# Performance work log

Measured on AMD Instinct MI355X. Metric: run time of the kernel, lower is better.

Reference implementation:

```python
import jax, jax.numpy as jnp
import numpy as np

HID = 64; H = 2; D = 32; L = 2; G = 64; F_IN = 771
NA = 120000; NE = 60000; E0 = 1500000; E1 = 1000000; E2 = 1000000


def _seg_mean(x, seg, n):
    s = jax.ops.segment_sum(x, seg, num_segments=n)
    c = jax.ops.segment_sum(jnp.ones((x.shape[0], 1), x.dtype), seg, num_segments=n)
    return s / jnp.maximum(c, 1.0)


def setup_inputs() -> dict:
    ks = jax.random.split(jax.random.key(0), 32)
    r = lambda i, s: 0.02 * jax.random.normal(ks[i], s, jnp.float32)
    z = lambda s: jnp.zeros(s, jnp.float32)
    inp = {}
    inp['x_argument'] = jax.random.normal(ks[0], (NA, F_IN), jnp.float32)
    inp['x_evidence'] = jax.random.normal(ks[1], (NE, F_IN), jnp.float32)
    inp['Win'] = r(2, (2, F_IN, HID)); inp['b_in'] = z((2, HID))
    inp['Wk'] = r(3, (L, 2, HID, HID)); inp['bk'] = z((L, 2, HID))
    inp['Wq'] = r(4, (L, 2, HID, HID)); inp['bq'] = z((L, 2, HID))
    inp['Wv'] = r(5, (L, 2, HID, HID)); inp['bv'] = z((L, 2, HID))
    inp['Wa'] = r(6, (L, 2, HID, HID)); inp['ba'] = z((L, 2, HID))
    inp['skip'] = jnp.ones((L, 2), jnp.float32)
    inp['Watt'] = r(7, (L, 3, H, D, D)); inp['Wmsg'] = r(8, (L, 3, H, D, D))
    inp['prel'] = jnp.ones((L, 3, H), jnp.float32)
    inp['Wnews'] = r(9, (384, HID)); inp['bnews'] = z((HID,))
    inp['Wdeb'] = r(10, (HID, HID)); inp['bdeb'] = z((HID,))
    inp['Wqm'] = r(11, (HID, HID)); inp['bqm'] = z((HID,))
    inp['Wkm'] = r(12, (HID, HID)); inp['bkm'] = z((HID,))
    inp['Wvm'] = r(13, (HID, HID)); inp['bvm'] = z((HID,))
    inp['Wom'] = r(14, (HID, HID)); inp['bom'] = z((HID,))
    inp['Wc1'] = r(15, (2 * HID, 64)); inp['bc1'] = z((64,))
    inp['Wc2'] = r(16, (64, 1)); inp['bc2'] = z((1,))
    inp['e0_src'] = jax.random.randint(ks[17], (E0,), 0, NA)
    inp['e0_dst'] = jax.random.randint(ks[18], (E0,), 0, NA)
    inp['e1_src'] = jax.random.randint(ks[19], (E1,), 0, NE)
    inp['e1_dst'] = jax.random.randint(ks[20], (E1,), 0, NA)
    inp['e2_src'] = jax.random.randint(ks[21], (E2,), 0, NA)
    inp['e2_dst'] = jax.random.randint(ks[22], (E2,), 0, NE)
    inp['batch_arg'] = jnp.sort(jax.random.randint(ks[23], (NA,), 0, G))
    return inp


def reference(x_argument, x_evidence, Win, b_in, Wk, bk, Wq, bq, Wv, bv, Wa, ba,
              skip, Watt, Wmsg, prel, Wnews, bnews, Wdeb, bdeb,
              Wqm, bqm, Wkm, bkm, Wvm, bvm, Wom, bom, Wc1, bc1, Wc2, bc2,
              e0_src, e0_dst, e1_src, e1_dst, e2_src, e2_dst, batch_arg):
    # Claim embedding from RAW features (slice 384:768), pooled per graph.
    claim_raw = _seg_mean(x_argument[:, 384:768], batch_arg, G)
    # Per-node-type input projection + ReLU. type 0 = argument, 1 = evidence.
    xs = [jax.nn.relu(x_argument @ Win[0] + b_in[0]),
          jax.nn.relu(x_evidence @ Win[1] + b_in[1])]
    # (src_type, dst_type, src_idx, dst_idx) for each heterogeneous edge type.
    edges = [(0, 0, e0_src, e0_dst), (1, 0, e1_src, e1_dst), (0, 1, e2_src, e2_dst)]
    scale = 1.0 / jnp.sqrt(jnp.float32(D))
    for l in range(L):  # HGTConv stack
        Kt = [(xs[t] @ Wk[l, t] + bk[l, t]).reshape(-1, H, D) for t in range(2)]
        Qt = [(xs[t] @ Wq[l, t] + bq[l, t]).reshape(-1, H, D) for t in range(2)]
        Vt = [(xs[t] @ Wv[l, t] + bv[l, t]).reshape(-1, H, D) for t in range(2)]
        buf = {0: [], 1: []}
        for e, (s, d, src, dst) in enumerate(edges):
            k2 = jnp.einsum('ehd,hdf->ehf', Kt[s][src], Watt[l, e])  # relation key transform
            v2 = jnp.einsum('ehd,hdf->ehf', Vt[s][src], Wmsg[l, e])  # relation msg transform
            sc = (Qt[d][dst] * k2).sum(-1) * prel[l, e] * scale      # (E, H)
            buf[d].append((sc, dst, v2))
        new_xs = []
        for d in range(2):
            n = xs[d].shape[0]
            sc = jnp.concatenate([b[0] for b in buf[d]], 0)
            dst = jnp.concatenate([b[1] for b in buf[d]], 0)
            v2 = jnp.concatenate([b[2] for b in buf[d]], 0)
            # segment softmax over all incoming edges of each destination node
            m = jax.ops.segment_max(sc, dst, num_segments=n)
            ex = jnp.exp(sc - m[dst])
            den = jax.ops.segment_sum(ex, dst, num_segments=n)
            alpha = ex / den[dst]
            agg = jax.ops.segment_sum(alpha[..., None] * v2, dst, num_segments=n).reshape(n, HID)
            out = jax.nn.gelu(agg, approximate=False) @ Wa[l, d] + ba[l, d]
            beta = jax.nn.sigmoid(skip[l, d])
            new_xs.append(beta * out + (1.0 - beta) * xs[d])
        xs = new_xs
    graph_emb = _seg_mean(xs[0], batch_arg, G)
    eF = claim_raw @ Wnews + bnews          # (G, HID)
    g = graph_emb @ Wdeb + bdeb             # (G, HID)
    # MultiheadAttention with query len 1 and key len 1: softmax over a single
    # key is identically 1, so attn_out == out_proj(v_proj(g)) exactly
    # (Wqm/bqm/Wkm/bkm receive exactly zero gradient, matching torch).
    v = g @ Wvm + bvm
    attn_out = v @ Wom + bom
    h = jax.nn.relu(jnp.concatenate([g, attn_out], -1) @ Wc1 + bc1)  # dropout is eval-mode identity
    return h @ Wc2 + bc2  # (G, 1)
```

## Files before the change

kernel.cpp:

```cpp
#include <hip/hip_runtime.h>
#include <math.h>

#define N0 120000
#define N1 60000
#define E0N 1500000
#define E1N 1000000
#define E2N 1000000
#define FIN 771
#define NG 64
#define KSTEPS_IN 25

#define GB0 ((N0 + 127) / 128)
#define GB1 ((N1 + 127) / 128)
#define AB0 ((N0 + 3) / 4)
#define AB1 ((N1 + 3) / 4)
#define SB0 ((N0 + 1023) / 1024)
#define SB1 ((N1 + 1023) / 1024)
#define PREPB 70

#define Q0O   ((size_t)0)
#define KV00O ((size_t)N0 * 128)
#define KV02O ((size_t)N0 * 256)
#define Q1O   ((size_t)N0 * 384)
#define KV11O ((size_t)N0 * 384 + (size_t)N1 * 128)

#define SKV 256.0f
#define INV_SKV 0.00390625f

typedef __attribute__((ext_vector_type(8))) short short8;
typedef __attribute__((ext_vector_type(4))) float f32x4;
typedef __attribute__((ext_vector_type(2))) float f32x2;
typedef float f32x4u __attribute__((ext_vector_type(4), aligned(4)));
typedef __attribute__((ext_vector_type(4))) unsigned short ushort4v;
typedef unsigned short ushort;
typedef unsigned char uchar;

__device__ __forceinline__ float gelu_f(float v) {
    return 0.5f * v * (1.f + erff(v * 0.70710678118654752f));
}
__device__ __forceinline__ ushort f2b(float f) {
    union { float f; unsigned u; } v; v.f = f;
    unsigned u = v.u;
    return (ushort)((u + 0x7FFFu + ((u >> 16) & 1u)) >> 16);
}
__device__ __forceinline__ float b2f(ushort h) {
    union { unsigned u; float f; } v; v.u = ((unsigned)h) << 16; return v.f;
}
__device__ __forceinline__ float lo16(unsigned u) {
    union { unsigned x; float f; } v; v.x = u << 16; return v.f;
}
__device__ __forceinline__ float hi16(unsigned u) {
    union { unsigned x; float f; } v; v.x = u & 0xFFFF0000u; return v.f;
}
__device__ __forceinline__ int asi(float f) { union { float f; int i; } v; v.f = f; return v.i; }
__device__ __forceinline__ float asf(int i) { union { int i; float f; } v; v.i = i; return v.f; }

__device__ __forceinline__ void proj_phase(
    const ushort* xls, char* scratch, int type, int l, int w, int lane, int tid,
    int r0b, int nrows,
    const ushort* __restrict__ Wpack, const float* __restrict__ bpack,
    uchar* __restrict__ projAll)
{
    short8 bfr[2][2];
    #pragma unroll
    for (int ksp = 0; ksp < 2; ++ksp)
        #pragma unroll
        for (int rb = 0; rb < 2; ++rb)
            bfr[ksp][rb] = *(const short8*)&xls[(w * 32 + rb * 16 + (lane & 15)) * 72
                                                + ksp * 32 + (lane >> 4) * 8];
    const int sbase = l * 8 + (type ? 5 : 0);
    const int c0b = (lane >> 4) * 4;
    const int ngroups = type ? 2 : 3;

    for (int grp = 0; grp < ngroups; ++grp) {
        const int s0 = (grp == 0) ? 0 : (grp * 2 - 1);
        const int nsl = (grp == 0) ? 1 : 2;
        for (int si = 0; si < nsl; ++si) {
            const int slot = s0 + si;
            const ushort* Wp = Wpack + (size_t)(sbase + slot) * 4096;
            const float* bias = bpack + (size_t)(sbase + slot) * 64;
            f32x4 acc[2][4] = {};
            #pragma unroll
            for (int ksp = 0; ksp < 2; ++ksp) {
                const ushort* wb = Wp + ksp * 2048 + lane * 8;
                #pragma unroll
                for (int cg = 0; cg < 4; ++cg) {
                    short8 afr = *(const short8*)&wb[cg * 512];
                    acc[0][cg] = __builtin_amdgcn_mfma_f32_16x16x32_bf16(afr, bfr[ksp][0], acc[0][cg], 0, 0, 0);
                    acc[1][cg] = __builtin_amdgcn_mfma_f32_16x16x32_bf16(afr, bfr[ksp][1], acc[1][cg], 0, 0, 0);
                }
            }
            #pragma unroll
            for (int rb = 0; rb < 2; ++rb) {
                int lrow = w * 32 + rb * 16 + (lane & 15);
                const int sw = (lrow & 7) << 4;
                #pragma unroll
                for (int cg = 0; cg < 4; ++cg) {
                    int c = cg * 16 + c0b;
                    float v0 = acc[rb][cg][0] + bias[c + 0];
                    float v1 = acc[rb][cg][1] + bias[c + 1];
                    float v2 = acc[rb][cg][2] + bias[c + 2];
                    float v3 = acc[rb][cg][3] + bias[c + 3];
                    if (grp == 0) {
                        ushort4v o;
                        o[0] = f2b(v0); o[1] = f2b(v1); o[2] = f2b(v2); o[3] = f2b(v3);
                        *(ushort4v*)(scratch + lrow * 128 + ((c * 2) ^ sw)) = o;
                    } else {
                        int wrd = __builtin_amdgcn_cvt_pk_fp8_f32(v0 * SKV, v1 * SKV, 0, 0);
                        wrd = __builtin_amdgcn_cvt_pk_fp8_f32(v2 * SKV, v3 * SKV, wrd, 1);
                        *(int*)(scratch + lrow * 128 + ((((c >> 2) << 3) + (si << 2)) ^ sw)) = wrd;
                    }
                }
            }
        }
        __syncthreads();
        size_t ooff;
        if (grp == 0) ooff = type ? Q1O : Q0O;
        else if (grp == 1) ooff = type ? KV11O : KV00O;
        else ooff = KV02O;
        char* outg = (char*)projAll + ooff + (size_t)r0b * 128;
        #pragma unroll
        for (int q = 0; q < 4; ++q) {
            int off = q * 4096 + tid * 16;
            int row = off >> 7;
            int inner = off & 127;
            if (r0b + row < nrows)
                *(uint4*)(outg + off) =
                    *(const uint4*)(scratch + row * 128 + (inner ^ ((row & 7) << 4)));
        }
        __syncthreads();
    }
}

__global__ __launch_bounds__(256) void inproj_proj_kernel(
    const float* __restrict__ xa, const float* __restrict__ xe,
    const ushort* __restrict__ Wpin, const float* __restrict__ b_in,
    ushort* __restrict__ xs0, ushort* __restrict__ xs1,
    const ushort* __restrict__ Wpack, const float* __restrict__ bpack,
    uchar* __restrict__ projAll)
{
    __shared__ ushort xls[128 * 72];
    __shared__ char scratch[16384];
    const int bx = blockIdx.x;
    const int type = (bx >= GB0) ? 1 : 0;
    const float* __restrict__ x = type ? xe : xa;
    const int nrows = type ? N1 : N0;
    const ushort* __restrict__ Wp = Wpin + (type ? (size_t)KSTEPS_IN * 2048 : 0);
    const float* __restrict__ bias = b_in + type * 64;
    ushort* __restrict__ out = type ? xs1 : xs0;

    const int tid = threadIdx.x, w = tid >> 6, lane = tid & 63;
    const int r0b = (type ? bx - GB0 : bx) * 128;

    const int rA = min(r0b + w * 32 + (lane & 15), nrows - 1);
    const int rB = min(r0b + w * 32 + 16 + (lane & 15), nrows - 1);
    const float* __restrict__ xA = x + (size_t)rA * FIN + (lane >> 4) * 8;
    const float* __restrict__ xB = x + (size_t)rB * FIN + (lane >> 4) * 8;

    f32x4 acc[2][4] = {};
    f32x4u cb[3][4];
    cb[0][0] = *(const f32x4u*)xA;        cb[0][1] = *(const f32x4u*)(xA + 4);
    cb[0][2] = *(const f32x4u*)xB;        cb[0][3] = *(const f32x4u*)(xB + 4);
    cb[1][0] = *(const f32x4u*)(xA + 32); cb[1][1] = *(const f32x4u*)(xA + 36);
    cb[1][2] = *(const f32x4u*)(xB + 32); cb[1][3] = *(const f32x4u*)(xB + 36);

    #pragma unroll
    for (int ks = 0; ks < 24; ++ks) {
        if (ks + 2 < 24) {
            const float* pA = xA + (ks + 2) * 32;
            const float* pB = xB + (ks + 2) * 32;
            cb[(ks + 2) % 3][0] = *(const f32x4u*)pA;
            cb[(ks + 2) % 3][1] = *(const f32x4u*)(pA + 4);
            cb[(ks + 2) % 3][2] = *(const f32x4u*)pB;
            cb[(ks + 2) % 3][3] = *(const f32x4u*)(pB + 4);
        }
        const int cur = ks % 3;
        short8 bA, bB;
        #pragma unroll
        for (int j = 0; j < 4; ++j) {
            bA[j]     = (short)f2b(cb[cur][0][j]);
            bA[j + 4] = (short)f2b(cb[cur][1][j]);
            bB[j]     = (short)f2b(cb[cur][2][j]);
            bB[j + 4] = (short)f2b(cb[cur][3][j]);
        }
        const ushort* wb = Wp + (size_t)ks * 2048 + lane * 8;
        #pragma unroll
        for (int cg = 0; cg < 4; ++cg) {
            short8 afr = *(const short8*)&wb[cg * 512];
            acc[0][cg] = __builtin_amdgcn_mfma_f32_16x16x32_bf16(afr, bA, acc[0][cg], 0, 0, 0);
            acc[1][cg] = __builtin_amdgcn_mfma_f32_16x16x32_bf16(afr, bB, acc[1][cg], 0, 0, 0);
        }
    }
    {
        short8 bA = {}, bB = {};
        if ((lane >> 4) == 0) {
            const float* tA = x + (size_t)rA * FIN + 768;
            const float* tB = x + (size_t)rB * FIN + 768;
            bA[0] = (short)f2b(tA[0]); bA[1] = (short)f2b(tA[1]); bA[2] = (short)f2b(tA[2]);
            bB[0] = (short)f2b(tB[0]); bB[1] = (short)f2b(tB[1]); bB[2] = (short)f2b(tB[2]);
        }
        const ushort* wb = Wp + (size_t)24 * 2048 + lane * 8;
        #pragma unroll
        for (int cg = 0; cg < 4; ++cg) {
            short8 afr = *(const short8*)&wb[cg * 512];
            acc[0][cg] = __builtin_amdgcn_mfma_f32_16x16x32_bf16(afr, bA, acc[0][cg], 0, 0, 0);
            acc[1][cg] = __builtin_amdgcn_mfma_f32_16x16x32_bf16(afr, bB, acc[1][cg], 0, 0, 0);
        }
    }
    const int c0b = (lane >> 4) * 4;
    #pragma unroll
    for (int rb = 0; rb < 2; ++rb) {
        int lrow = w * 32 + rb * 16 + (lane & 15);
        int r = r0b + lrow;
        #pragma unroll
        for (int cg = 0; cg < 4; ++cg) {
            int c = cg * 16 + c0b;
            ushort4v h;
            h[0] = f2b(fmaxf(acc[rb][cg][0] + bias[c + 0], 0.f));
            h[1] = f2b(fmaxf(acc[rb][cg][1] + bias[c + 1], 0.f));
            h[2] = f2b(fmaxf(acc[rb][cg][2] + bias[c + 2], 0.f));
            h[3] = f2b(fmaxf(acc[rb][cg][3] + bias[c + 3], 0.f));
            *(ushort4v*)&xls[lrow * 72 + c] = h;
            if (r < nrows) *(ushort4v*)&out[(size_t)r * 64 + c] = h;
        }
    }
    __syncthreads();
    proj_phase(xls, scratch, type, 0, w, lane, tid, r0b, nrows, Wpack, bpack, projAll);
}

template <int DO_PROJ>
__global__ __launch_bounds__(256) void epi_kernel(
    const float* __restrict__ agg0, const float* __restrict__ agg1,
    const ushort* __restrict__ WaPack, const float* __restrict__ ba,
    ushort* __restrict__ xs0, ushort* __restrict__ xs1,
    const float* __restrict__ skip, int l,
    const ushort* __restrict__ Wpack, const float* __restrict__ bpack,
    uchar* __restrict__ projAll)
{
    __shared__ ushort xls[DO_PROJ ? 128 * 72 : 64];
    __shared__ char scratch[DO_PROJ ? 16384 : 64];
    const int bx = blockIdx.x;
    const int type = (bx >= GB0) ? 1 : 0;
    const float* __restrict__ in = type ? agg1 : agg0;
    ushort* __restrict__ xs = type ? xs1 : xs0;
    const int nrows = type ? N1 : N0;
    const ushort* __restrict__ Wp = WaPack + (size_t)(l * 2 + type) * 4096;
    const float* __restrict__ bias = ba + (size_t)(l * 2 + type) * 64;
    const float beta = 1.f / (1.f + __expf(-skip[l * 2 + type]));

    const int tid = threadIdx.x, w = tid >> 6, lane = tid & 63;
    const int r0b = (type ? bx - GB0 : bx) * 128;
    const int r0 = r0b + w * 32;
    f32x4 acc[2][4] = {};
    #pragma unroll
    for (int ksp = 0; ksp < 2; ++ksp) {
        short8 bfr[2];
        #pragma unroll
        for (int rb = 0; rb < 2; ++rb) {
            int gr = min(r0 + rb * 16 + (lane & 15), nrows - 1);
            const float* src = in + (size_t)gr * 64 + ksp * 32 + (lane >> 4) * 8;
            float4 f0 = *(const float4*)src;
            float4 f1 = *(const float4*)(src + 4);
            short8 t;
            t[0] = (short)f2b(gelu_f(f0.x)); t[1] = (short)f2b(gelu_f(f0.y));
            t[2] = (short)f2b(gelu_f(f0.z)); t[3] = (short)f2b(gelu_f(f0.w));
            t[4] = (short)f2b(gelu_f(f1.x)); t[5] = (short)f2b(gelu_f(f1.y));
            t[6] = (short)f2b(gelu_f(f1.z)); t[7] = (short)f2b(gelu_f(f1.w));
            bfr[rb] = t;
        }
        const ushort* wb = Wp + ksp * 2048 + lane * 8;
        #pragma unroll
        for (int cg = 0; cg < 4; ++cg) {
            short8 afr = *(const short8*)&wb[cg * 512];
            acc[0][cg] = __builtin_amdgcn_mfma_f32_16x16x32_bf16(afr, bfr[0], acc[0][cg], 0, 0, 0);
            acc[1][cg] = __builtin_amdgcn_mfma_f32_16x16x32_bf16(afr, bfr[1], acc[1][cg], 0, 0, 0);
        }
    }
    const int c0b = (lane >> 4) * 4;
    #pragma unroll
    for (int rb = 0; rb < 2; ++rb) {
        int lrow = w * 32 + rb * 16 + (lane & 15);
        int r = r0b + lrow;
        int gr = min(r, nrows - 1);
        #pragma unroll
        for (int cg = 0; cg < 4; ++cg) {
            int c = cg * 16 + c0b;
            ushort4v xo = *(const ushort4v*)&xs[(size_t)gr * 64 + c];
            ushort4v h;
            h[0] = f2b(beta * (acc[rb][cg][0] + bias[c + 0]) + (1.f - beta) * b2f(xo[0]));
            h[1] = f2b(beta * (acc[rb][cg][1] + bias[c + 1]) + (1.f - beta) * b2f(xo[1]));
            h[2] = f2b(beta * (acc[rb][cg][2] + bias[c + 2]) + (1.f - beta) * b2f(xo[2]));
            h[3] = f2b(beta * (acc[rb][cg][3] + bias[c + 3]) + (1.f - beta) * b2f(xo[3]));
            if (DO_PROJ) *(ushort4v*)&xls[lrow * 72 + c] = h;
            if (r < nrows) *(ushort4v*)&xs[(size_t)r * 64 + c] = h;
        }
    }
    if (DO_PROJ) {
        __syncthreads();
        proj_phase(xls, scratch, type, l + 1, w, lane, tid, r0b, nrows, Wpack, bpack, projAll);
    }
}

__global__ __launch_bounds__(256) void prep_zero_kernel(
    const float* __restrict__ Wq, const float* __restrict__ bq,
    const float* __restrict__ Wk, const float* __restrict__ bk,
    const float* __restrict__ Wv, const float* __restrict__ bv,
    const float* __restrict__ Watt, const float* __restrict__ Wmsg,
    const float* __restrict__ prel, const float* __restrict__ Win,
    const float* __restrict__ Wa,
    ushort* __restrict__ Wpack, float* __restrict__ bpack,
    ushort* __restrict__ Wpin, ushort* __restrict__ WaPack,
    int* __restrict__ c0, int* __restrict__ c1,
    int* __restrict__ gs, int* __restrict__ gc)
{
    __shared__ float WF[4096];
    const int b = blockIdx.x;
    const int tid = threadIdx.x;
    if (b >= PREPB) {
        int i = (b - PREPB) * 256 + tid;
        if (i < N0) c0[i] = 0;
        else if (i < N0 + N1) c1[i - N0] = 0;
        else if (i < N0 + N1 + NG * 64) gs[i - N0 - N1] = 0;
        else if (i < N0 + N1 + NG * 64 + NG) gc[i - N0 - N1 - NG * 64] = 0;
        return;
    }
    if (b < 16) {
        const int l = b >> 3;
        const int slot = b & 7;
        const float SCALE = 0.17677669529663689f;
        ushort* outW = Wpack + (size_t)(l * 8 + slot) * 4096;
        float* outB = bpack + (size_t)(l * 8 + slot) * 64;
        const float *Wsrc = 0, *bsrc = 0, *A = 0, *prelE = 0;
        int copy = 0;
        switch (slot) {
            case 0: Wsrc = Wq + (l*2+0)*4096; bsrc = bq + (l*2+0)*64; copy = 1; break;
            case 5: Wsrc = Wq + (l*2+1)*4096; bsrc = bq + (l*2+1)*64; copy = 1; break;
            case 1: Wsrc = Wk + (l*2+0)*4096; bsrc = bk + (l*2+0)*64; A = Watt + (l*3+0)*2048; prelE = prel + l*6 + 0; break;
            case 2: Wsrc = Wv + (l*2+0)*4096; bsrc = bv + (l*2+0)*64; A = Wmsg + (l*3+0)*2048; break;
            case 3: Wsrc = Wk + (l*2+0)*4096; bsrc = bk + (l*2+0)*64; A = Watt + (l*3+2)*2048; prelE = prel + l*6 + 4; break;
            case 4: Wsrc = Wv + (l*2+0)*4096; bsrc = bv + (l*2+0)*64; A = Wmsg + (l*3+2)*2048; break;
            case 6: Wsrc = Wk + (l*2+1)*4096; bsrc = bk + (l*2+1)*64; A = Watt + (l*3+1)*2048; prelE = prel + l*6 + 2; break;
            case 7: Wsrc = Wv + (l*2+1)*4096; bsrc = bv + (l*2+1)*64; A = Wmsg + (l*3+1)*2048; break;
        }
        if (copy) {
            for (int idx = tid; idx < 4096; idx += 256) WF[idx] = Wsrc[idx];
            if (tid < 64) outB[tid] = bsrc[tid];
        } else {
            for (int idx = tid; idx < 4096; idx += 256) {
                int k = idx >> 6, c = idx & 63, h = c >> 5, f = c & 31;
                float s = 0.f;
                for (int d = 0; d < 32; ++d)
                    s += Wsrc[k * 64 + h * 32 + d] * A[(h * 32 + d) * 32 + f];
                if (prelE) s *= prelE[h] * SCALE;
                WF[idx] = s;
            }
            if (tid < 64) {
                int h = tid >> 5, f = tid & 31;
                float s = 0.f;
                for (int d = 0; d < 32; ++d)
                    s += bsrc[h * 32 + d] * A[(h * 32 + d) * 32 + f];
                if (prelE) s *= prelE[h] * SCALE;
                outB[tid] = s;
            }
        }
        __syncthreads();
        for (int idx = tid; idx < 4096; idx += 256) {
            int ksp = idx >> 11, rem = idx & 2047;
            int cg = rem >> 9, rem2 = rem & 511;
            int lane = rem2 >> 3, j = rem2 & 7;
            int k = ksp * 32 + (lane >> 4) * 8 + j;
            int c = cg * 16 + (lane & 15);
            outW[idx] = f2b(WF[k * 64 + c]);
        }
    } else if (b < 16 + 2 * KSTEPS_IN) {
        const int pb = b - 16;
        const int type = pb / KSTEPS_IN, ks = pb % KSTEPS_IN;
        const float* W = Win + (size_t)type * FIN * 64;
        ushort* out = Wpin + (size_t)pb * 2048;
        for (int idx = tid; idx < 2048; idx += 256) {
            int cg = idx >> 9, rem = idx & 511, lane = rem >> 3, j = rem & 7;
            int k = ks * 32 + (lane >> 4) * 8 + j;
            int c = cg * 16 + (lane & 15);
            out[idx] = f2b((k < FIN) ? W[(size_t)k * 64 + c] : 0.f);
        }
    } else {
        const int mb = b - 16 - 2 * KSTEPS_IN;
        const float* W = Wa + (size_t)mb * 4096;
        ushort* o = WaPack + (size_t)mb * 4096;
        for (int idx = tid; idx < 4096; idx += 256) {
            int ksp = idx >> 11, rem = idx & 2047;
            int cg = rem >> 9, rem2 = rem & 511;
            int lane = rem2 >> 3, j = rem2 & 7;
            int k = ksp * 32 + (lane >> 4) * 8 + j;
            int c = cg * 16 + (lane & 15);
            o[idx] = f2b(W[k * 64 + c]);
        }
    }
}

__global__ void hist_all_kernel(
    const int* __restrict__ e0d, const int* __restrict__ e1d, const int* __restrict__ e2d,
    int* __restrict__ cnt0, int* __restrict__ cnt1)
{
    const int Q0 = E0N / 4, Q1 = E1N / 4, Q2 = E2N / 4;
    const int total = Q0 + Q1 + Q2;
    for (int i = blockIdx.x * blockDim.x + threadIdx.x; i < total; i += gridDim.x * blockDim.x) {
        int4 d;
        int* cnt;
        if (i < Q0) { d = *(const int4*)(e0d + i * 4); cnt = cnt0; }
        else if (i < Q0 + Q1) { d = *(const int4*)(e1d + (i - Q0) * 4); cnt = cnt0; }
        else { d = *(const int4*)(e2d + (i - Q0 - Q1) * 4); cnt = cnt1; }
        atomicAdd(&cnt[d.x], 1);
        atomicAdd(&cnt[d.y], 1);
        atomicAdd(&cnt[d.z], 1);
        atomicAdd(&cnt[d.w], 1);
    }
}

__global__ __launch_bounds__(256) void scan1_all_kernel(
    int* __restrict__ cnt0, int* __restrict__ cnt1,
    int* __restrict__ off0, int* __restrict__ off1,
    int* __restrict__ bsA, int* __restrict__ bsB)
{
    __shared__ int sa[256], sb[256];
    const int tid = threadIdx.x;
    const int b = blockIdx.x;
    int* cnt; int n; int* off; int* bsum; int lb;
    if (b < SB0) { cnt = cnt0; n = N0; off = off0; bsum = bsA; lb = b; }
    else { cnt = cnt1; n = N1; off = off1; bsum = bsB; lb = b - SB0; }
    const int base = lb * 1024 + tid * 4;
    int v[4];
    int run = 0;
    #pragma unroll
    for (int i = 0; i < 4; ++i) {
        int x = (base + i < n) ? cnt[base + i] : 0;
        run += x; v[i] = run;
    }
    #pragma unroll
    for (int i = 0; i < 4; ++i)
        if (base + i < n) cnt[base + i] = 0;
    sa[tid] = run;
    __syncthreads();
    int* src = sa; int* dst = sb;
    for (int d = 1; d < 256; d <<= 1) {
        int x = src[tid];
        if (tid >= d) x += src[tid - d];
        dst[tid] = x;
        __syncthreads();
        int* t = src; src = dst; dst = t;
    }
    int excl = src[tid] - run;
    #pragma unroll
    for (int i = 0; i < 4; ++i)
        if (base + i < n) off[base + i + 1] = excl + v[i];
    if (tid == 255) bsum[lb] = src[255];
}

__global__ __launch_bounds__(256) void scan3_all_kernel(
    int* __restrict__ off0, int* __restrict__ off1,
    const int* __restrict__ bsA, const int* __restrict__ bsB)
{
    __shared__ int red[256];
    const int b = blockIdx.x;
    const int tid = threadIdx.x;
    int* off; const int* bsum; int n; int lb;
    if (b < SB0) { off = off0; bsum = bsA; n = N0; lb = b; }
    else { off = off1; bsum = bsB; n = N1; lb = b - SB0; }
    int partial = 0;
    for (int i = tid; i < lb; i += 256) partial += bsum[i];
    red[tid] = partial;
    __syncthreads();
    #pragma unroll
    for (int d = 128; d > 0; d >>= 1) {
        if (tid < d) red[tid] += red[tid + d];
        __syncthreads();
    }
    const int add = red[0];
    const int base = lb * 1024 + tid * 4;
    #pragma unroll
    for (int i = 0; i < 4; ++i)
        if (base + i < n) off[base + i + 1] += add;
    if (lb == 0 && tid == 0) off[0] = 0;
}

__global__ void scatter_all_kernel(
    const int* __restrict__ e0s, const int* __restrict__ e0d,
    const int* __restrict__ e1s, const int* __restrict__ e1d,
    const int* __restrict__ e2s, const int* __restrict__ e2d,
    const int* __restrict__ off0, const int* __restrict__ off1,
    int* __restrict__ cnt0, int* __restrict__ cnt1,
    int* __restrict__ rec0, int* __restrict__ rec1)
{
    const int Q0 = E0N / 4, Q1 = E1N / 4, Q2 = E2N / 4;
    const int total = Q0 + Q1 + Q2;
    for (int i = blockIdx.x * blockDim.x + threadIdx.x; i < total; i += gridDim.x * blockDim.x) {
        int4 d, sv;
        const int* off; int* cnt; int* rec; int tag;
        if (i < Q0) {
            d = *(const int4*)(e0d + i * 4); sv = *(const int4*)(e0s + i * 4);
            off = off0; cnt = cnt0; rec = rec0; tag = 0;
        } else if (i < Q0 + Q1) {
            int k = (i - Q0) * 4;
            d = *(const int4*)(e1d + k); sv = *(const int4*)(e1s + k);
            off = off0; cnt = cnt0; rec = rec0; tag = 1 << 20;
        } else {
            int k = (i - Q0 - Q1) * 4;
            d = *(const int4*)(e2d + k); sv = *(const int4*)(e2s + k);
            off = off1; cnt = cnt1; rec = rec1; tag = 0;
        }
        rec[off[d.x] + atomicAdd(&cnt[d.x], 1)] = sv.x | tag;
        rec[off[d.y] + atomicAdd(&cnt[d.y], 1)] = sv.y | tag;
        rec[off[d.z] + atomicAdd(&cnt[d.z], 1)] = sv.z | tag;
        rec[off[d.w] + atomicAdd(&cnt[d.w], 1)] = sv.w | tag;
    }
}

__global__ __launch_bounds__(256) void agg_fused(
    const int* __restrict__ off0, const int* __restrict__ rec0,
    const int* __restrict__ off1, const int* __restrict__ rec1,
    const uchar* __restrict__ projAll,
    float* __restrict__ agg0, float* __restrict__ agg1)
{
    const int bx = blockIdx.x;
    const int type = (bx >= AB0) ? 1 : 0;
    const int lane = threadIdx.x & 63;
    const int node = (type ? bx - AB0 : bx) * 4 + (threadIdx.x >> 6);
    const int ndst = type ? N1 : N0;
    if (node >= ndst) return;
    const int* __restrict__ off = type ? off1 : off0;
    const int* __restrict__ rec = type ? rec1 : rec0;
    const ushort* __restrict__ Q = (const ushort*)(projAll + (type ? Q1O : Q0O));
    const uchar* __restrict__ KVa = projAll + (type ? KV02O : KV00O);
    const uchar* __restrict__ KVb = projAll + (type ? KV02O : KV11O);
    float* __restrict__ outAgg = type ? agg1 : agg0;

    const int grp = lane >> 4;
    const int gi  = lane & 15;
    float q0, q1, q2, q3;
    {
        const unsigned* qp = (const unsigned*)(Q + (size_t)node * 64 + gi * 4);
        unsigned u0 = qp[0], u1 = qp[1];
        q0 = lo16(u0) * INV_SKV; q1 = hi16(u0) * INV_SKV;
        q2 = lo16(u1) * INV_SKV; q3 = hi16(u1) * INV_SKV;
    }
    const int s = off[node], e = off[node + 1];
    float den = 0.f, a0 = 0.f, a1 = 0.f, a2 = 0.f, a3 = 0.f;
    for (int j = s; j < e; j += 16) {
        bool v[4]; uint2 kv[4]; float p[4];
        #pragma unroll
        for (int q = 0; q < 4; ++q) {
            int jj = j + grp + q * 4;
            v[q] = jj < e;
            int r = rec[v[q] ? jj : s];
            const uchar* KV = (r & (1 << 20)) ? KVb : KVa;
            kv[q] = *(const uint2*)(KV + ((size_t)(unsigned)(r & 0xFFFFF) << 7) + gi * 8);
        }
        #pragma unroll
        for (int q = 0; q < 4; ++q) {
            f32x2 kA = __builtin_amdgcn_cvt_pk_f32_fp8(kv[q].x, 0);
            f32x2 kB = __builtin_amdgcn_cvt_pk_f32_fp8(kv[q].x, 1);
            p[q] = kA[0] * q0 + kA[1] * q1 + kB[0] * q2 + kB[1] * q3;
        }
        #pragma unroll
        for (int q = 0; q < 4; ++q) p[q] += asf(__builtin_amdgcn_ds_swizzle(asi(p[q]), 0x041F));
        #pragma unroll
        for (int q = 0; q < 4; ++q) p[q] += asf(__builtin_amdgcn_ds_swizzle(asi(p[q]), 0x081F));
        #pragma unroll
        for (int q = 0; q < 4; ++q) p[q] += asf(__builtin_amdgcn_ds_swizzle(asi(p[q]), 0x101F));
        #pragma unroll
        for (int q = 0; q < 4; ++q) {
            float wgt = v[q] ? __expf(p[q]) : 0.f;
            den += wgt;
            f32x2 vA = __builtin_amdgcn_cvt_pk_f32_fp8(kv[q].y, 0);
            f32x2 vB = __builtin_amdgcn_cvt_pk_f32_fp8(kv[q].y, 1);
            a0 = fmaf(wgt, vA[0], a0);
            a1 = fmaf(wgt, vA[1], a1);
            a2 = fmaf(wgt, vB[0], a2);
            a3 = fmaf(wgt, vB[1], a3);
        }
    }
    a0 += __shfl_xor(a0, 16); a0 += __shfl_xor(a0, 32);
    a1 += __shfl_xor(a1, 16); a1 += __shfl_xor(a1, 32);
    a2 += __shfl_xor(a2, 16); a2 += __shfl_xor(a2, 32);
    a3 += __shfl_xor(a3, 16); a3 += __shfl_xor(a3, 32);
    den += __shfl_xor(den, 16); den += __shfl_xor(den, 32);
    if (lane < 16) {
        float inv = (den > 0.f) ? 1.f / (den * SKV) : 0.f;
        float4 o;
        o.x = a0 * inv; o.y = a1 * inv; o.z = a2 * inv; o.w = a3 * inv;
        *(float4*)&outAgg[(size_t)node * 64 + gi * 4] = o;
    }
}

__global__ __launch_bounds__(256) void segsum_kernel(
    const ushort* __restrict__ xs, const int* __restrict__ seg, int n,
    float* __restrict__ gsum, int* __restrict__ gcnt)
{
    const int lane = threadIdx.x & 63;
    const int wid = blockIdx.x * 4 + (threadIdx.x >> 6);
    const int rbeg = wid * 256;
    if (rbeg >= n) return;
    const int rend = min(rbeg + 256, n);
    float s = 0.f;
    int cur = seg[rbeg];
    int run = 0;
    for (int r = rbeg; r < rend; ++r) {
        int sg = seg[r];
        if (sg != cur) {
            atomicAdd(&gsum[cur * 64 + lane], s);
            if (lane == 0) atomicAdd(&gcnt[cur], run);
            cur = sg; s = 0.f; run = 0;
        }
        s += b2f(xs[(size_t)r * 64 + lane]);
        run++;
    }
    atomicAdd(&gsum[cur * 64 + lane], s);
    if (lane == 0) atomicAdd(&gcnt[cur], run);
}

__global__ __launch_bounds__(256) void head_kernel(
    const float* __restrict__ gsum, const int* __restrict__ gcnt,
    const float* __restrict__ Wdeb, const float* __restrict__ bdeb,
    const float* __restrict__ Wvm, const float* __restrict__ bvm,
    const float* __restrict__ Wom, const float* __restrict__ bom,
    const float* __restrict__ Wc1, const float* __restrict__ bc1,
    const float* __restrict__ Wc2, const float* __restrict__ bc2,
    float* __restrict__ outp)
{
    __shared__ float A[4096], B[4096], C[4096];
    const int tid = threadIdx.x;
    for (int idx = tid; idx < 4096; idx += 256) {
        int g = idx >> 6;
        A[idx] = gsum[idx] / fmaxf((float)gcnt[g], 1.f);
    }
    __syncthreads();
    for (int idx = tid; idx < 4096; idx += 256) {
        int g = idx >> 6, c = idx & 63;
        float s = bdeb[c];
        for (int k = 0; k < 64; ++k) s = fmaf(A[g * 64 + k], Wdeb[k * 64 + c], s);
        B[idx] = s;
    }
    __syncthreads();
    for (int idx = tid; idx < 4096; idx += 256) {
        int g = idx >> 6, c = idx & 63;
        float s = bvm[c];
        for (int k = 0; k < 64; ++k) s = fmaf(B[g * 64 + k], Wvm[k * 64 + c], s);
        C[idx] = s;
    }
    __syncthreads();
    for (int idx = tid; idx < 4096; idx += 256) {
        int g = idx >> 6, c = idx & 63;
        float s = bom[c];
        for (int k = 0; k < 64; ++k) s = fmaf(C[g * 64 + k], Wom[k * 64 + c], s);
        A[idx] = s;
    }
    __syncthreads();
    for (int idx = tid; idx < 4096; idx += 256) {
        int g = idx >> 6, c = idx & 63;
        float s = bc1[c];
        for (int k = 0; k < 64; ++k) s = fmaf(B[g * 64 + k], Wc1[k * 64 + c], s);
        for (int k = 0; k < 64; ++k) s = fmaf(A[g * 64 + k], Wc1[(64 + k) * 64 + c], s);
        C[idx] = fmaxf(s, 0.f);
    }
    __syncthreads();
    if (tid < 64) {
        float s = bc2[0];
        for (int c = 0; c < 64; ++c) s = fmaf(C[tid * 64 + c], Wc2[c], s);
        outp[tid] = s;
    }
}

extern "C" void kernel_launch(void* const* d_in, const int* in_sizes, int n_in,
                              void* d_out, int out_size, void* d_ws, size_t ws_size,
                              hipStream_t stream)
{
    const float* x_arg = (const float*)d_in[0];
    const float* x_ev  = (const float*)d_in[1];
    const float* Win   = (const float*)d_in[2];
    const float* b_in  = (const float*)d_in[3];
    const float* Wk    = (const float*)d_in[4];
    const float* bk    = (const float*)d_in[5];
    const float* Wq    = (const float*)d_in[6];
    const float* bq    = (const float*)d_in[7];
    const float* Wv    = (const float*)d_in[8];
    const float* bv    = (const float*)d_in[9];
    const float* Wa    = (const float*)d_in[10];
    const float* ba    = (const float*)d_in[11];
    const float* skip  = (const float*)d_in[12];
    const float* Watt  = (const float*)d_in[13];
    const float* Wmsg  = (const float*)d_in[14];
    const float* prel  = (const float*)d_in[15];
    const float* Wdeb  = (const float*)d_in[18];
    const float* bdeb  = (const float*)d_in[19];
    const float* Wvm   = (const float*)d_in[24];
    const float* bvm   = (const float*)d_in[25];
    const float* Wom   = (const float*)d_in[26];
    const float* bom   = (const float*)d_in[27];
    const float* Wc1   = (const float*)d_in[28];
    const float* bc1   = (const float*)d_in[29];
    const float* Wc2   = (const float*)d_in[30];
    const float* bc2   = (const float*)d_in[31];
    const int* e0s = (const int*)d_in[32];
    const int* e0d = (const int*)d_in[33];
    const int* e1s = (const int*)d_in[34];
    const int* e1d = (const int*)d_in[35];
    const int* e2s = (const int*)d_in[36];
    const int* e2d = (const int*)d_in[37];
    const int* batch = (const int*)d_in[38];
    float* outp = (float*)d_out;

    char* w = (char*)d_ws;
    size_t o = 0;
    auto alloc = [&](size_t bytes) -> char* {
        char* p = w + o;
        o = (o + bytes + 255) & ~(size_t)255;
        return p;
    };
    ushort* xs0  = (ushort*)alloc((size_t)N0 * 64 * 2);
    ushort* xs1  = (ushort*)alloc((size_t)N1 * 64 * 2);
    uchar* projAll = (uchar*)alloc((size_t)N0 * 384 + (size_t)N1 * 256);
    float* agg0  = (float*)alloc((size_t)N0 * 64 * 4);
    float* agg1  = (float*)alloc((size_t)N1 * 64 * 4);
    int* off0 = (int*)alloc((size_t)(N0 + 1) * 4);
    int* off1 = (int*)alloc((size_t)(N1 + 1) * 4);
    int* cnt0 = (int*)alloc((size_t)N0 * 4);
    int* cnt1 = (int*)alloc((size_t)N1 * 4);
    int* rec0 = (int*)alloc((size_t)(E0N + E1N) * 4);
    int* rec1 = (int*)alloc((size_t)E2N * 4);
    int* bsA  = (int*)alloc(256 * 4);
    int* bsB  = (int*)alloc(256 * 4);
    ushort* Wpack = (ushort*)alloc((size_t)16 * 4096 * 2);
    float* bpack = (float*)alloc((size_t)16 * 64 * 4);
    ushort* Wpin = (ushort*)alloc((size_t)2 * KSTEPS_IN * 2048 * 2);
    ushort* WaPack = (ushort*)alloc((size_t)4 * 4096 * 2);
    float* gsum = (float*)alloc((size_t)NG * 64 * 4);
    int* gcnt = (int*)alloc((size_t)NG * 4);
    if (o > ws_size) return;

    const int ZB = (N0 + N1 + NG * 64 + NG + 255) / 256;

    prep_zero_kernel<<<PREPB + ZB, 256, 0, stream>>>(
        Wq, bq, Wk, bk, Wv, bv, Watt, Wmsg, prel, Win, Wa,
        Wpack, bpack, Wpin, WaPack, cnt0, cnt1, (int*)gsum, gcnt);
    hist_all_kernel<<<1024, 256, 0, stream>>>(e0d, e1d, e2d, cnt0, cnt1);
    scan1_all_kernel<<<SB0 + SB1, 256, 0, stream>>>(cnt0, cnt1, off0, off1, bsA, bsB);
    scan3_all_kernel<<<SB0 + SB1, 256, 0, stream>>>(off0, off1, bsA, bsB);
    scatter_all_kernel<<<1024, 256, 0, stream>>>(
        e0s, e0d, e1s, e1d, e2s, e2d, off0, off1, cnt0, cnt1, rec0, rec1);
    inproj_proj_kernel<<<GB0 + GB1, 256, 0, stream>>>(
        x_arg, x_ev, Wpin, b_in, xs0, xs1, Wpack, bpack, projAll);
    agg_fused<<<AB0 + AB1, 256, 0, stream>>>(off0, rec0, off1, rec1, projAll, agg0, agg1);
    epi_kernel<1><<<GB0 + GB1, 256, 0, stream>>>(
        agg0, agg1, WaPack, ba, xs0, xs1, skip, 0, Wpack, bpack, projAll);
    agg_fused<<<AB0 + AB1, 256, 0, stream>>>(off0, rec0, off1, rec1, projAll, agg0, agg1);
    epi_kernel<0><<<GB0 + GB1, 256, 0, stream>>>(
        agg0, agg1, WaPack, ba, xs0, xs1, skip, 1, Wpack, bpack, projAll);
    {
        int waves = (N0 + 255) / 256;
        segsum_kernel<<<(waves + 3) / 4, 256, 0, stream>>>(xs0, batch, N0, gsum, gcnt);
    }
    head_kernel<<<1, 256, 0, stream>>>(gsum, gcnt, Wdeb, bdeb, Wvm, bvm, Wom, bom,
                                       Wc1, bc1, Wc2, bc2, outp);
}
```

Baseline: 974.9 us.

## Stage input-projection rows through LDS with coalesced loads, halve block rows

The input projection kernel now loads each block's contiguous slab of fp32 input rows with fully coalesced vector loads, converts them to bf16, and stores them in a shared-memory tile before the MFMA loop. Previously each lane read strided 32-byte chunks per row directly from global memory. Blocks now cover 64 rows instead of 128, and proj_phase is templated on the row count. The aim is better DRAM efficiency on the large 771-wide input read and more blocks in flight. The cost is about 99KB of LDS per block, which limits occupancy, plus an extra sync.

Measured after the change: 1.040 ms. 1.07x slower.

```diff
diff --git a/kernel.cpp b/kernel.cpp
--- a/kernel.cpp
+++ b/kernel.cpp
@@ -12,6 +12,8 @@
 
 #define GB0 ((N0 + 127) / 128)
 #define GB1 ((N1 + 127) / 128)
+#define GB064 (N0 / 64)
+#define GB164 ((N1 + 63) / 64)
 #define AB0 ((N0 + 3) / 4)
 #define AB1 ((N1 + 3) / 4)
 #define SB0 ((N0 + 1023) / 1024)
@@ -55,18 +57,20 @@
 __device__ __forceinline__ int asi(float f) { union { float f; int i; } v; v.f = f; return v.i; }
 __device__ __forceinline__ float asf(int i) { union { int i; float f; } v; v.i = i; return v.f; }
 
+template <int NRB>
 __device__ __forceinline__ void proj_phase(
     const ushort* xls, char* scratch, int type, int l, int w, int lane, int tid,
     int r0b, int nrows,
     const ushort* __restrict__ Wpack, const float* __restrict__ bpack,
     uchar* __restrict__ projAll)
 {
-    short8 bfr[2][2];
+    const int ROWS = NRB * 64;
+    short8 bfr[2][NRB];
     #pragma unroll
     for (int ksp = 0; ksp < 2; ++ksp)
         #pragma unroll
-        for (int rb = 0; rb < 2; ++rb)
-            bfr[ksp][rb] = *(const short8*)&xls[(w * 32 + rb * 16 + (lane & 15)) * 72
+        for (int rb = 0; rb < NRB; ++rb)
+            bfr[ksp][rb] = *(const short8*)&xls[(w * 16 * NRB + rb * 16 + (lane & 15)) * 72
                                                 + ksp * 32 + (lane >> 4) * 8];
     const int sbase = l * 8 + (type ? 5 : 0);
     const int c0b = (lane >> 4) * 4;
@@ -79,20 +83,21 @@
             const int slot = s0 + si;
             const ushort* Wp = Wpack + (size_t)(sbase + slot) * 4096;
             const float* bias = bpack + (size_t)(sbase + slot) * 64;
-            f32x4 acc[2][4] = {};
+            f32x4 acc[NRB][4] = {};
             #pragma unroll
             for (int ksp = 0; ksp < 2; ++ksp) {
                 const ushort* wb = Wp + ksp * 2048 + lane * 8;
                 #pragma unroll
                 for (int cg = 0; cg < 4; ++cg) {
                     short8 afr = *(const short8*)&wb[cg * 512];
-                    acc[0][cg] = __builtin_amdgcn_mfma_f32_16x16x32_bf16(afr, bfr[ksp][0], acc[0][cg], 0, 0, 0);
-                    acc[1][cg] = __builtin_amdgcn_mfma_f32_16x16x32_bf16(afr, bfr[ksp][1], acc[1][cg], 0, 0, 0);
+                    #pragma unroll
+                    for (int rb = 0; rb < NRB; ++rb)
+                        acc[rb][cg] = __builtin_amdgcn_mfma_f32_16x16x32_bf16(afr, bfr[ksp][rb], acc[rb][cg], 0, 0, 0);
                 }
             }
             #pragma unroll
-            for (int rb = 0; rb < 2; ++rb) {
-                int lrow = w * 32 + rb * 16 + (lane & 15);
+            for (int rb = 0; rb < NRB; ++rb) {
+                int lrow = w * 16 * NRB + rb * 16 + (lane & 15);
                 const int sw = (lrow & 7) << 4;
                 #pragma unroll
                 for (int cg = 0; cg < 4; ++cg) {
@@ -120,7 +125,7 @@
         else ooff = KV02O;
         char* outg = (char*)projAll + ooff + (size_t)r0b * 128;
         #pragma unroll
-        for (int q = 0; q < 4; ++q) {
+        for (int q = 0; q < ROWS / 32; ++q) {
             int off = q * 4096 + tid * 16;
             int row = off >> 7;
             int inner = off & 127;
@@ -139,10 +144,12 @@
     const ushort* __restrict__ Wpack, const float* __restrict__ bpack,
     uchar* __restrict__ projAll)
 {
-    __shared__ ushort xls[128 * 72];
-    __shared__ char scratch[16384];
+    __shared__ union {
+        ushort xt[64 * 772];
+        struct { ushort xls[64 * 72]; char scratch[8192]; } pp;
+    } sm;
     const int bx = blockIdx.x;
-    const int type = (bx >= GB0) ? 1 : 0;
+    const int type = (bx >= GB064) ? 1 : 0;
     const float* __restrict__ x = type ? xe : xa;
     const int nrows = type ? N1 : N0;
     const ushort* __restrict__ Wp = Wpin + (type ? (size_t)KSTEPS_IN * 2048 : 0);
@@ -150,82 +157,85 @@
     ushort* __restrict__ out = type ? xs1 : xs0;
 
     const int tid = threadIdx.x, w = tid >> 6, lane = tid & 63;
-    const int r0b = (type ? bx - GB0 : bx) * 128;
-
-    const int rA = min(r0b + w * 32 + (lane & 15), nrows - 1);
-    const int rB = min(r0b + w * 32 + 16 + (lane & 15), nrows - 1);
-    const float* __restrict__ xA = x + (size_t)rA * FIN + (lane >> 4) * 8;
-    const float* __restrict__ xB = x + (size_t)rB * FIN + (lane >> 4) * 8;
-
-    f32x4 acc[2][4] = {};
-    f32x4u cb[3][4];
-    cb[0][0] = *(const f32x4u*)xA;        cb[0][1] = *(const f32x4u*)(xA + 4);
-    cb[0][2] = *(const f32x4u*)xB;        cb[0][3] = *(const f32x4u*)(xB + 4);
-    cb[1][0] = *(const f32x4u*)(xA + 32); cb[1][1] = *(const f32x4u*)(xA + 36);
-    cb[1][2] = *(const f32x4u*)(xB + 32); cb[1][3] = *(const f32x4u*)(xB + 36);
-
+    const int r0b = (type ? bx - GB064 : bx) * 64;
+
+    const float* __restrict__ src = x + (size_t)r0b * FIN;
+    const int nelem = (min(r0b + 64, nrows) - r0b) * FIN;
+    int e = tid * 4;
+    int row = (e >= FIN) ? 1 : 0;
+    int col = e - row * FIN;
+    for (int b = 0; b < 6; ++b) {
+        f32x4u v[8];
+        #pragma unroll
+        for (int i = 0; i < 8; ++i) {
+            int ee = e + i * 1024;
+            v[i] = (ee < nelem) ? *(const f32x4u*)(src + ee) : (f32x4u){};
+        }
+        #pragma unroll
+        for (int i = 0; i < 8; ++i) {
+            #pragma unroll
+            for (int j = 0; j < 4; ++j) {
+                int cc = col + j, rr = row;
+                if (cc >= FIN) { cc -= FIN; ++rr; }
+                sm.xt[rr * 772 + cc] = f2b(v[i][j]);
+            }
+            row += 1; col += 253;
+            if (col >= FIN) { col -= FIN; row += 1; }
+        }
+        e += 8192;
+    }
+    if (tid < 48) {
+        int ee = 49152 + tid * 4;
+        f32x4u v = (ee < nelem) ? *(const f32x4u*)(src + ee) : (f32x4u){};
+        int cc = ee - 63 * FIN;
+        #pragma unroll
+        for (int j = 0; j < 4; ++j) sm.xt[63 * 772 + cc + j] = f2b(v[j]);
+    }
+    __syncthreads();
+
+    const int mrow = w * 16 + (lane & 15);
+    f32x4 acc[4] = {};
     #pragma unroll
     for (int ks = 0; ks < 24; ++ks) {
-        if (ks + 2 < 24) {
-            const float* pA = xA + (ks + 2) * 32;
-            const float* pB = xB + (ks + 2) * 32;
-            cb[(ks + 2) % 3][0] = *(const f32x4u*)pA;
-            cb[(ks + 2) % 3][1] = *(const f32x4u*)(pA + 4);
-            cb[(ks + 2) % 3][2] = *(const f32x4u*)pB;
-            cb[(ks + 2) % 3][3] = *(const f32x4u*)(pB + 4);
-        }
-        const int cur = ks % 3;
-        short8 bA, bB;
-        #pragma unroll
-        for (int j = 0; j < 4; ++j) {
-            bA[j]     = (short)f2b(cb[cur][0][j]);
-            bA[j + 4] = (short)f2b(cb[cur][1][j]);
-            bB[j]     = (short)f2b(cb[cur][2][j]);
-            bB[j + 4] = (short)f2b(cb[cur][3][j]);
-        }
+        short8 bfr = *(const short8*)&sm.xt[mrow * 772 + ks * 32 + (lane >> 4) * 8];
         const ushort* wb = Wp + (size_t)ks * 2048 + lane * 8;
         #pragma unroll
         for (int cg = 0; cg < 4; ++cg) {
             short8 afr = *(const short8*)&wb[cg * 512];
-            acc[0][cg] = __builtin_amdgcn_mfma_f32_16x16x32_bf16(afr, bA, acc[0][cg], 0, 0, 0);
-            acc[1][cg] = __builtin_amdgcn_mfma_f32_16x16x32_bf16(afr, bB, acc[1][cg], 0, 0, 0);
+            acc[cg] = __builtin_amdgcn_mfma_f32_16x16x32_bf16(afr, bfr, acc[cg], 0, 0, 0);
         }
     }
     {
-        short8 bA = {}, bB = {};
+        short8 bfr = {};
         if ((lane >> 4) == 0) {
-            const float* tA = x + (size_t)rA * FIN + 768;
-            const float* tB = x + (size_t)rB * FIN + 768;
-            bA[0] = (short)f2b(tA[0]); bA[1] = (short)f2b(tA[1]); bA[2] = (short)f2b(tA[2]);
-            bB[0] = (short)f2b(tB[0]); bB[1] = (short)f2b(tB[1]); bB[2] = (short)f2b(tB[2]);
+            bfr[0] = (short)sm.xt[mrow * 772 + 768];
+            bfr[1] = (short)sm.xt[mrow * 772 + 769];
+            bfr[2] = (short)sm.xt[mrow * 772 + 770];
         }
         const ushort* wb = Wp + (size_t)24 * 2048 + lane * 8;
         #pragma unroll
         for (int cg = 0; cg < 4; ++cg) {
             short8 afr = *(const short8*)&wb[cg * 512];
-            acc[0][cg] = __builtin_amdgcn_mfma_f32_16x16x32_bf16(afr, bA, acc[0][cg], 0, 0, 0);
-            acc[1][cg] = __builtin_amdgcn_mfma_f32_16x16x32_bf16(afr, bB, acc[1][cg], 0, 0, 0);
-        }
-    }
+            acc[cg] = __builtin_amdgcn_mfma_f32_16x16x32_bf16(afr, bfr, acc[cg], 0, 0, 0);
+        }
+    }
+    __syncthreads();
+
     const int c0b = (lane >> 4) * 4;
-    #pragma unroll
-    for (int rb = 0; rb < 2; ++rb) {
-        int lrow = w * 32 + rb * 16 + (lane & 15);
-        int r = r0b + lrow;
-        #pragma unroll
-        for (int cg = 0; cg < 4; ++cg) {
-            int c = cg * 16 + c0b;
-            ushort4v h;
-            h[0] = f2b(fmaxf(acc[rb][cg][0] + bias[c + 0], 0.f));
-            h[1] = f2b(fmaxf(acc[rb][cg][1] + bias[c + 1], 0.f));
-            h[2] = f2b(fmaxf(acc[rb][cg][2] + bias[c + 2], 0.f));
-            h[3] = f2b(fmaxf(acc[rb][cg][3] + bias[c + 3], 0.f));
-            *(ushort4v*)&xls[lrow * 72 + c] = h;
-            if (r < nrows) *(ushort4v*)&out[(size_t)r * 64 + c] = h;
-        }
-    }
-    __syncthreads();
-    proj_phase(xls, scratch, type, 0, w, lane, tid, r0b, nrows, Wpack, bpack, projAll);
+    const int r = r0b + mrow;
+    #pragma unroll
+    for (int cg = 0; cg < 4; ++cg) {
+        int c = cg * 16 + c0b;
+        ushort4v h;
+        h[0] = f2b(fmaxf(acc[cg][0] + bias[c + 0], 0.f));
+        h[1] = f2b(fmaxf(acc[cg][1] + bias[c + 1], 0.f));
+        h[2] = f2b(fmaxf(acc[cg][2] + bias[c + 2], 0.f));
+        h[3] = f2b(fmaxf(acc[cg][3] + bias[c + 3], 0.f));
+        *(ushort4v*)&sm.pp.xls[mrow * 72 + c] = h;
+        if (r < nrows) *(ushort4v*)&out[(size_t)r * 64 + c] = h;
+    }
+    __syncthreads();
+    proj_phase<1>(sm.pp.xls, sm.pp.scratch, type, 0, w, lane, tid, r0b, nrows, Wpack, bpack, projAll);
 }
 
 template <int DO_PROJ>
@@ -297,7 +307,7 @@
     }
     if (DO_PROJ) {
         __syncthreads();
-        proj_phase(xls, scratch, type, l + 1, w, lane, tid, r0b, nrows, Wpack, bpack, projAll);
+        proj_phase<2>(xls, scratch, type, l + 1, w, lane, tid, r0b, nrows, Wpack, bpack, projAll);
     }
 }
 
@@ -747,7 +757,7 @@
     scan3_all_kernel<<<SB0 + SB1, 256, 0, stream>>>(off0, off1, bsA, bsB);
     scatter_all_kernel<<<1024, 256, 0, stream>>>(
         e0s, e0d, e1s, e1d, e2s, e2d, off0, off1, cnt0, cnt1, rec0, rec1);
-    inproj_proj_kernel<<<GB0 + GB1, 256, 0, stream>>>(
+    inproj_proj_kernel<<<GB064 + GB164, 256, 0, stream>>>(
         x_arg, x_ev, Wpin, b_in, xs0, xs1, Wpack, bpack, projAll);
     agg_fused<<<AB0 + AB1, 256, 0, stream>>>(off0, rec0, off1, rec1, projAll, agg0, agg1);
     epi_kernel<1><<<GB0 + GB1, 256, 0, stream>>>(
```
